# Kernel optimization log

Hardware: AMD Instinct MI355X
Metric: run time of the kernel (lower is better)

The kernel has to match this reference:

```python
import jax, jax.numpy as jnp
import numpy as np
import math

NEG = -1e9
NUM_SQUEEZE = 2


def seq_mask(lengths, max_len, dtype):
    return (jnp.arange(max_len)[None, :] < lengths[:, None]).astype(dtype)


def maximum_path(logp, attn_mask, x_lengths, y_lengths):
    """Monotonic alignment search (Viterbi DP). logp, attn_mask: [B, Tx, Ty]."""
    B, Tx, Ty = logp.shape
    logp = jnp.where(attn_mask > 0, logp, NEG)
    cols = jnp.moveaxis(logp, 2, 0)  # [Ty, B, Tx]

    v0 = jnp.where(jnp.arange(Tx)[None, :] == 0, 0.0, NEG).astype(logp.dtype)
    v0 = jnp.broadcast_to(v0, (B, Tx))

    def fwd(v, col):
        v_shift = jnp.concatenate([jnp.full((B, 1), NEG, logp.dtype), v[:, :-1]], axis=1)
        v_new = col + jnp.maximum(v, v_shift)
        return v_new, v_new

    _, values = jax.lax.scan(fwd, v0, cols)  # [Ty, B, Tx] DP table

    def bwd(index, j):
        active = j < y_lengths  # [B]
        row = jax.nn.one_hot(index, Tx, dtype=logp.dtype) * active[:, None].astype(logp.dtype)
        vprev = values[jnp.maximum(j - 1, 0)]  # [B, Tx]
        v_here = jnp.take_along_axis(vprev, index[:, None], axis=1)[:, 0]
        v_left = jnp.take_along_axis(vprev, jnp.maximum(index - 1, 0)[:, None], axis=1)[:, 0]
        dec = (index != 0) & ((index == j) | (v_here < v_left)) & active & (j > 0)
        return jnp.where(dec, index - 1, index), row

    js = jnp.arange(Ty - 1, -1, -1)
    _, rows = jax.lax.scan(bwd, x_lengths - 1, js)  # reversed j order
    path = jnp.moveaxis(jnp.flip(rows, 0), 0, 2)  # [B, Tx, Ty]
    return path * attn_mask


def setup_inputs() -> dict:
    key = jax.random.key(0)
    ks = jax.random.split(key, 6)
    B, C, Ten, Tde = 32, 80, 512, 2048
    return {
        "o_mean": jax.random.normal(ks[0], (B, C, Ten), jnp.float32),
        "o_log_scale": jax.random.normal(ks[1], (B, C, Ten), jnp.float32) * 0.1,
        "o_dur_log": jax.random.normal(ks[2], (B, 1, Ten), jnp.float32),
        "z": jax.random.normal(ks[3], (B, C, Tde), jnp.float32),
        "x_lengths": jax.random.randint(ks[4], (B,), Ten // 2, Ten + 1, jnp.int32),
        "y_lengths": jax.random.randint(ks[5], (B,), Tde // 2, Tde + 1, jnp.int32),
    }


def reference(o_mean, o_log_scale, o_dur_log, z, x_lengths, y_lengths):
    B, C, Ten = o_mean.shape
    Tde = z.shape[2]
    dt = o_mean.dtype

    # preprocess: floor y_lengths to multiple of num_squeeze
    y_lengths = (y_lengths // NUM_SQUEEZE) * NUM_SQUEEZE

    x_mask = seq_mask(x_lengths, Ten, dt)[:, None, :]   # [B,1,Tx]
    y_mask = seq_mask(y_lengths, Tde, dt)[:, None, :]   # [B,1,Ty]
    attn_mask = x_mask[:, 0, :, None] * y_mask[:, 0, None, :]  # [B,Tx,Ty]

    z = z * y_mask  # decoder output is masked

    # log-likelihood terms (torch.no_grad in original)
    o_scale = jnp.exp(-2.0 * o_log_scale)                       # [B,C,Tx]
    logp1 = jnp.sum(-0.5 * math.log(2 * math.pi) - o_log_scale, axis=1)[:, :, None]
    logp2 = jnp.einsum('bct,bcs->bts', o_scale, -0.5 * z * z)   # [B,Tx,Ty]
    logp3 = jnp.einsum('bct,bcs->bts', o_mean * o_scale, z)
    logp4 = jnp.sum(-0.5 * o_mean * o_mean * o_scale, axis=1)[:, :, None]
    logp = logp1 + logp2 + logp3 + logp4

    attn = maximum_path(logp, attn_mask, x_lengths, y_lengths)  # [B,Tx,Ty] hard path

    # compute_outputs
    y_mean = jnp.einsum('bts,bct->bcs', attn, o_mean)           # [B,C,Ty]
    y_log_scale = jnp.einsum('bts,bct->bcs', attn, o_log_scale)
    o_attn_dur = jnp.log1p(jnp.sum(attn, axis=-1))[:, None, :] * x_mask  # [B,1,Tx]

    return (
        jnp.transpose(z, (0, 2, 1)),            # z: [B,Ty,C]
        jnp.transpose(y_mean, (0, 2, 1)),       # y_mean: [B,Ty,C]
        jnp.transpose(y_log_scale, (0, 2, 1)),  # y_log_scale: [B,Ty,C]
        jnp.transpose(attn, (0, 2, 1)),         # alignments: [B,Ty,Tx]
        jnp.transpose(o_dur_log, (0, 2, 1)),    # durations_log: [B,Tx,1]
        jnp.transpose(o_attn_dur, (0, 2, 1)),   # total_durations_log: [B,Tx,1]
    )
```

## Files before the change

kernel.cpp:

```cpp
#include <hip/hip_runtime.h>
#include <math.h>

#define BB  32
#define CC  80
#define TXX 512
#define TYY 2048
#define NEGV -1e9f

__global__ __launch_bounds__(256) void k_prep(
    const float* __restrict__ om, const float* __restrict__ ols,
    float* __restrict__ SA, float* __restrict__ SB,
    float* __restrict__ L1, float* __restrict__ L4,
    float* __restrict__ OMTf, float* __restrict__ OLSTf,
    int* __restrict__ DUR)
{
    int gid = blockIdx.x * 256 + threadIdx.x;
    int b = gid >> 9, t = gid & 511;
    const float* pm = om  + (size_t)b * CC * TXX + t;
    const float* pl = ols + (size_t)b * CC * TXX + t;
    float l1 = 0.f, l4 = 0.f;
    for (int c = 0; c < CC; ++c) {
        float m  = pm[(size_t)c * TXX];
        float ls = pl[(size_t)c * TXX];
        float sa = expf(-2.0f * ls);
        l1 += (-0.9189385332046727f - ls);
        l4 += ((-0.5f * m) * m) * sa;
        SA[((size_t)b * CC + c) * TXX + t] = sa;
        SB[((size_t)b * CC + c) * TXX + t] = m * sa;
        OMTf [((size_t)b * TXX + t) * CC + c] = m;
        OLSTf[((size_t)b * TXX + t) * CC + c] = ls;
    }
    L1[gid] = l1; L4[gid] = l4; DUR[gid] = 0;
}

__global__ __launch_bounds__(256) void k_logp(
    const float* __restrict__ SA, const float* __restrict__ SB,
    const float* __restrict__ L1, const float* __restrict__ L4,
    const float* __restrict__ z,
    const int* __restrict__ xlp, const int* __restrict__ ylp,
    float* __restrict__ logp)
{
    int b = blockIdx.z;
    int ylen = (ylp[b] >> 1) << 1;
    int s0 = blockIdx.y * 128;
    if (s0 >= ylen) return;
    int t0 = blockIdx.x * 64;
    int xlen = xlp[b];
    int tid = threadIdx.x;

    __shared__ float sA[16][64], sB[16][64], sZ[16][128], sW[16][128];

    float acc2[4][8], acc3[4][8];
    #pragma unroll
    for (int i = 0; i < 4; ++i)
        #pragma unroll
        for (int j = 0; j < 8; ++j) { acc2[i][j] = 0.f; acc3[i][j] = 0.f; }

    int tt = (tid & 15) << 2;
    int ss = (tid >> 4) << 3;
    int r  = tid >> 4;
    int c4 = (tid & 15) << 2;
    int s8 = (tid & 15) << 3;

    for (int c0 = 0; c0 < CC; c0 += 16) {
        const float* pa = SA + ((size_t)b * CC + (c0 + r)) * TXX + t0 + c4;
        const float* pb = SB + ((size_t)b * CC + (c0 + r)) * TXX + t0 + c4;
        float4 va = *(const float4*)pa;
        float4 vb = *(const float4*)pb;
        *(float4*)&sA[r][c4] = va;
        *(float4*)&sB[r][c4] = vb;

        const float* pz = z + ((size_t)b * CC + (c0 + r)) * TYY + s0 + s8;
        float4 q0 = *(const float4*)pz;
        float4 q1 = *(const float4*)(pz + 4);
        float zf[8] = {q0.x, q0.y, q0.z, q0.w, q1.x, q1.y, q1.z, q1.w};
        #pragma unroll
        for (int i = 0; i < 8; ++i) {
            sZ[r][s8 + i] = zf[i];
            sW[r][s8 + i] = (-0.5f * zf[i]) * zf[i];
        }
        __syncthreads();
        #pragma unroll
        for (int kc = 0; kc < 16; ++kc) {
            float4 a2 = *(const float4*)&sA[kc][tt];
            float4 a3 = *(const float4*)&sB[kc][tt];
            float4 z0 = *(const float4*)&sZ[kc][ss];
            float4 z1 = *(const float4*)&sZ[kc][ss + 4];
            float4 w0 = *(const float4*)&sW[kc][ss];
            float4 w1 = *(const float4*)&sW[kc][ss + 4];
            float av2[4] = {a2.x, a2.y, a2.z, a2.w};
            float av3[4] = {a3.x, a3.y, a3.z, a3.w};
            float bz[8]  = {z0.x, z0.y, z0.z, z0.w, z1.x, z1.y, z1.z, z1.w};
            float bw[8]  = {w0.x, w0.y, w0.z, w0.w, w1.x, w1.y, w1.z, w1.w};
            #pragma unroll
            for (int i = 0; i < 4; ++i)
                #pragma unroll
                for (int j = 0; j < 8; ++j) {
                    acc2[i][j] = fmaf(av2[i], bw[j], acc2[i][j]);
                    acc3[i][j] = fmaf(av3[i], bz[j], acc3[i][j]);
                }
        }
        __syncthreads();
    }

    float l1a[4], l4a[4]; int bad[4];
    #pragma unroll
    for (int i = 0; i < 4; ++i) {
        int t = t0 + tt + i;
        l1a[i] = L1[b * TXX + t];
        l4a[i] = L4[b * TXX + t];
        bad[i] = (t >= xlen);
    }
    #pragma unroll
    for (int j = 0; j < 8; ++j) {
        int s = s0 + ss + j;
        float vals[4];
        #pragma unroll
        for (int i = 0; i < 4; ++i) {
            float v = ((l1a[i] + acc2[i][j]) + acc3[i][j]) + l4a[i];
            vals[i] = bad[i] ? NEGV : v;
        }
        float4 o; o.x = vals[0]; o.y = vals[1]; o.z = vals[2]; o.w = vals[3];
        *(float4*)&logp[((size_t)b * TYY + s) * TXX + t0 + tt] = o;
    }
}

__device__ __forceinline__ void dp_step(float v[8], float4 c0, float4 c1,
                                        int s_abs, int lane, unsigned char* browBase)
{
    float left = __shfl_up(v[7], 1, 64);
    if (lane == 0) left = NEGV;
    if (s_abs >= 1) {
        unsigned by = 0u;
        by |= (v[0] < left) ? 1u   : 0u;
        by |= (v[1] < v[0]) ? 2u   : 0u;
        by |= (v[2] < v[1]) ? 4u   : 0u;
        by |= (v[3] < v[2]) ? 8u   : 0u;
        by |= (v[4] < v[3]) ? 16u  : 0u;
        by |= (v[5] < v[4]) ? 32u  : 0u;
        by |= (v[6] < v[5]) ? 64u  : 0u;
        by |= (v[7] < v[6]) ? 128u : 0u;
        browBase[(size_t)(s_abs - 1) * 64] = (unsigned char)by;
    }
    float m0 = fmaxf(v[0], left);
    float m1 = fmaxf(v[1], v[0]);
    float m2 = fmaxf(v[2], v[1]);
    float m3 = fmaxf(v[3], v[2]);
    float m4 = fmaxf(v[4], v[3]);
    float m5 = fmaxf(v[5], v[4]);
    float m6 = fmaxf(v[6], v[5]);
    float m7 = fmaxf(v[7], v[6]);
    v[0] = c0.x + m0; v[1] = c0.y + m1; v[2] = c0.z + m2; v[3] = c0.w + m3;
    v[4] = c1.x + m4; v[5] = c1.y + m5; v[6] = c1.z + m6; v[7] = c1.w + m7;
}

__global__ __launch_bounds__(64) void k_fwd(
    const float* __restrict__ logp, const int* __restrict__ ylp,
    unsigned char* __restrict__ BITS)
{
    int b = blockIdx.x, lane = threadIdx.x;
    int n = (ylp[b] >> 1) << 1;
    const float* lp = logp + (size_t)b * TYY * TXX + lane * 8;
    unsigned char* brow = BITS + (size_t)b * TYY * 64 + lane;
    float v[8];
    #pragma unroll
    for (int k = 0; k < 8; ++k) v[k] = NEGV;
    if (lane == 0) v[0] = 0.0f;

    float4 p0[8], p1[8];
    #pragma unroll
    for (int i = 0; i < 8; ++i) {
        int r = (i < n) ? i : (n - 1);
        p0[i] = *(const float4*)(lp + (size_t)r * TXX);
        p1[i] = *(const float4*)(lp + (size_t)r * TXX + 4);
    }
    int s = 0;
    while (s + 8 <= n) {
        #pragma unroll
        for (int u = 0; u < 8; ++u) {
            float4 c0 = p0[u], c1 = p1[u];
            int pr = s + 8; if (pr > n - 1) pr = n - 1;
            p0[u] = *(const float4*)(lp + (size_t)pr * TXX);
            p1[u] = *(const float4*)(lp + (size_t)pr * TXX + 4);
            dp_step(v, c0, c1, s, lane, brow);
            ++s;
        }
    }
    while (s < n) {
        float4 c0 = *(const float4*)(lp + (size_t)s * TXX);
        float4 c1 = *(const float4*)(lp + (size_t)s * TXX + 4);
        dp_step(v, c0, c1, s, lane, brow);
        ++s;
    }
}

__global__ __launch_bounds__(64) void k_bwd(
    const unsigned char* __restrict__ BITS, const int* __restrict__ xlp,
    const int* __restrict__ ylp, int* __restrict__ TSTAR, int* __restrict__ DUR)
{
    int b = blockIdx.x, lane = threadIdx.x;
    int ylen = (ylp[b] >> 1) << 1;
    int xlen = xlp[b];
    const unsigned char* bb = BITS + (size_t)b * TYY * 64;
    int* tst = TSTAR + b * TYY;
    int idx = xlen - 1;
    int j0 = ylen - 1;
    while (j0 >= 0) {
        int steps = (j0 + 1 < 32) ? (j0 + 1) : 32;
        int row = j0 - 1 - lane;
        int bw = idx >> 5; if (bw > 0) --bw;
        int base_bit = bw << 5;
        unsigned w0 = 0u, w1 = 0u;
        if (lane < steps && row >= 0) {
            const unsigned* rp = (const unsigned*)(bb + (size_t)row * 64);
            w0 = rp[bw]; w1 = rp[bw + 1];
        }
        unsigned long long wq = (((unsigned long long)w1) << 32) | w0;
        int saved = 0;
        #pragma unroll
        for (int k = 0; k < 32; ++k) {
            if (k >= steps) break;
            int j = j0 - k;
            if (lane == k) saved = idx;
            unsigned long long wk = __shfl(wq, k, 64);
            unsigned bit = (unsigned)(wk >> (idx - base_bit)) & 1u;
            int dec = (idx != 0 && j > 0 && (idx == j || bit)) ? 1 : 0;
            idx -= dec;
        }
        if (lane < steps) {
            tst[j0 - lane] = saved;
            atomicAdd(&DUR[b * TXX + saved], 1);
        }
        j0 -= steps;
    }
}

__global__ __launch_bounds__(256) void k_small(
    const float* __restrict__ odur, const int* __restrict__ xlp,
    const int* __restrict__ DUR, float* __restrict__ out4,
    float* __restrict__ out5)
{
    int gid = blockIdx.x * 256 + threadIdx.x;
    int b = gid >> 9, t = gid & 511;
    out4[gid] = odur[gid];
    int xlen = xlp[b];
    float d = (float)DUR[gid];
    out5[gid] = (t < xlen) ? log1pf(d) : 0.0f;
}

__global__ __launch_bounds__(256) void k_out_sc(
    const float* __restrict__ z, const float* __restrict__ OMTf,
    const float* __restrict__ OLSTf, const int* __restrict__ TSTAR,
    const int* __restrict__ ylp,
    float* __restrict__ out0, float* __restrict__ out1,
    float* __restrict__ out2)
{
    int b = blockIdx.y;
    int s0 = blockIdx.x * 32;
    int tid = threadIdx.x;
    int ylen = (ylp[b] >> 1) << 1;
    __shared__ int sT[32];
    __shared__ float zt[32][81];
    if (tid < 32) {
        int s = s0 + tid;
        sT[tid] = (s < ylen) ? TSTAR[b * TYY + s] : 0;
    }
    int c_l = tid >> 5, s_l = tid & 31;
    #pragma unroll
    for (int cp = 0; cp < 10; ++cp) {
        int c = cp * 8 + c_l;
        zt[s_l][c] = z[((size_t)b * CC + c) * TYY + s0 + s_l];
    }
    __syncthreads();
    for (int e = tid; e < 32 * 80; e += 256) {
        int sl = e / 80;
        int cc = e - sl * 80;
        int s = s0 + sl;
        bool valid = s < ylen;
        int t = sT[sl];
        size_t o = ((size_t)b * TYY + s) * 80 + cc;
        size_t g = ((size_t)b * TXX + t) * 80 + cc;
        out0[o] = valid ? zt[sl][cc] : 0.0f;
        out1[o] = valid ? OMTf[g]    : 0.0f;
        out2[o] = valid ? OLSTf[g]   : 0.0f;
    }
}

__global__ __launch_bounds__(256) void k_attn(
    const int* __restrict__ TSTAR, const int* __restrict__ ylp,
    float* __restrict__ out3)
{
    int b = blockIdx.y;
    int s0 = blockIdx.x * 16;
    int tid = threadIdx.x;
    int ylen = (ylp[b] >> 1) << 1;
    #pragma unroll
    for (int r = 0; r < 16; ++r) {
        int s = s0 + r;
        int tr = (s < ylen) ? TSTAR[b * TYY + s] : -1;
        int t = tid << 1;
        float2 val;
        val.x = (t == tr) ? 1.0f : 0.0f;
        val.y = (t + 1 == tr) ? 1.0f : 0.0f;
        ((float2*)(out3 + ((size_t)b * TYY + s) * TXX))[tid] = val;
    }
}

extern "C" void kernel_launch(void* const* d_in, const int* in_sizes, int n_in,
                              void* d_out, int out_size, void* d_ws, size_t ws_size,
                              hipStream_t stream)
{
    const float* om   = (const float*)d_in[0];
    const float* ols  = (const float*)d_in[1];
    const float* odur = (const float*)d_in[2];
    const float* z    = (const float*)d_in[3];
    const int* xl = (const int*)d_in[4];
    const int* yl = (const int*)d_in[5];

    float* out0 = (float*)d_out;
    float* out1 = out0 + 5242880;
    float* out2 = out0 + 10485760;
    float* out3 = out0 + 15728640;
    float* out4 = out0 + 49283072;
    float* out5 = out0 + 49299456;

    float* SA   = out0;
    float* SB   = out0 + 1310720;
    float* logp = out3;

    char* ws = (char*)d_ws;
    float* L1 = (float*)ws;
    float* L4 = (float*)(ws + 65536);
    float* OMTf  = (float*)(ws + 131072);
    float* OLSTf = (float*)(ws + 5373952);
    unsigned char* BITS = (unsigned char*)(ws + 10616832);
    int* TSTAR = (int*)(ws + 14811136);
    int* DUR   = (int*)(ws + 15073280);

    hipLaunchKernelGGL(k_prep, dim3(64), dim3(256), 0, stream,
                       om, ols, SA, SB, L1, L4, OMTf, OLSTf, DUR);
    hipLaunchKernelGGL(k_logp, dim3(8, 16, 32), dim3(256), 0, stream,
                       SA, SB, L1, L4, z, xl, yl, logp);
    hipLaunchKernelGGL(k_fwd, dim3(32), dim3(64), 0, stream, logp, yl, BITS);
    hipLaunchKernelGGL(k_bwd, dim3(32), dim3(64), 0, stream, BITS, xl, yl, TSTAR, DUR);
    hipLaunchKernelGGL(k_small, dim3(64), dim3(256), 0, stream, odur, xl, DUR, out4, out5);
    hipLaunchKernelGGL(k_out_sc, dim3(64, 32), dim3(256), 0, stream,
                       z, OMTf, OLSTf, TSTAR, yl, out0, out1, out2);
    hipLaunchKernelGGL(k_attn, dim3(128, 32), dim3(256), 0, stream, TSTAR, yl, out3);
}
```

Measured before the change: 769.4 us.

## Stage prep transposes in LDS, pack FMAs, buffer DP bits and deepen prefetch

k_prep now runs on a 2D grid and stages om/ols tiles in shared memory, so the transposed OMTf/OLSTf writes become coalesced instead of strided per-thread stores. k_logp keeps its accumulators as 2-wide vectors and uses elementwise FMA, aiming at packed FP32 FMA instructions. k_fwd doubles the logp prefetch depth to 16 rows and writes the per-step decision bytes to a shared ring buffer, then flushes them to global memory as wide coalesced uint4 stores. The cost is more shared memory and more complex index handling, which adds risk at the block boundaries and in the tail loop.

```diff
diff --git a/kernel.cpp b/kernel.cpp
--- a/kernel.cpp
+++ b/kernel.cpp
@@ -6,6 +6,8 @@
 #define TXX 512
 #define TYY 2048
 #define NEGV -1e9f
+
+typedef float v2f __attribute__((ext_vector_type(2)));
 
 __global__ __launch_bounds__(256) void k_prep(
     const float* __restrict__ om, const float* __restrict__ ols,
@@ -14,23 +16,40 @@
     float* __restrict__ OMTf, float* __restrict__ OLSTf,
     int* __restrict__ DUR)
 {
-    int gid = blockIdx.x * 256 + threadIdx.x;
-    int b = gid >> 9, t = gid & 511;
-    const float* pm = om  + (size_t)b * CC * TXX + t;
-    const float* pl = ols + (size_t)b * CC * TXX + t;
-    float l1 = 0.f, l4 = 0.f;
-    for (int c = 0; c < CC; ++c) {
-        float m  = pm[(size_t)c * TXX];
-        float ls = pl[(size_t)c * TXX];
+    int b = blockIdx.y;
+    int t0 = blockIdx.x * 64;
+    int tid = threadIdx.x;
+    int cl = tid >> 6;
+    int tl = tid & 63;
+    __shared__ float sm[64][81], sl[64][81], ssa[64][81];
+    #pragma unroll
+    for (int cp = 0; cp < 20; ++cp) {
+        int c = cp * 4 + cl;
+        size_t gidx = ((size_t)b * CC + c) * TXX + t0 + tl;
+        float m = om[gidx], ls = ols[gidx];
         float sa = expf(-2.0f * ls);
-        l1 += (-0.9189385332046727f - ls);
-        l4 += ((-0.5f * m) * m) * sa;
-        SA[((size_t)b * CC + c) * TXX + t] = sa;
-        SB[((size_t)b * CC + c) * TXX + t] = m * sa;
-        OMTf [((size_t)b * TXX + t) * CC + c] = m;
-        OLSTf[((size_t)b * TXX + t) * CC + c] = ls;
-    }
-    L1[gid] = l1; L4[gid] = l4; DUR[gid] = 0;
+        SA[gidx] = sa;
+        SB[gidx] = m * sa;
+        sm[tl][c] = m; sl[tl][c] = ls; ssa[tl][c] = sa;
+    }
+    __syncthreads();
+    if (tid < 64) {
+        float l1 = 0.f, l4 = 0.f;
+        #pragma unroll 4
+        for (int c = 0; c < CC; ++c) {
+            float m = sm[tid][c], ls = sl[tid][c], sa = ssa[tid][c];
+            l1 += (-0.9189385332046727f - ls);
+            l4 += ((-0.5f * m) * m) * sa;
+        }
+        int g = b * TXX + t0 + tid;
+        L1[g] = l1; L4[g] = l4; DUR[g] = 0;
+    }
+    size_t obase = (size_t)b * TXX * CC + (size_t)t0 * CC;
+    for (int e = tid; e < 64 * CC; e += 256) {
+        int t = e / CC, c = e - t * CC;
+        OMTf[obase + e]  = sm[t][c];
+        OLSTf[obase + e] = sl[t][c];
+    }
 }
 
 __global__ __launch_bounds__(256) void k_logp(
@@ -50,11 +69,11 @@
 
     __shared__ float sA[16][64], sB[16][64], sZ[16][128], sW[16][128];
 
-    float acc2[4][8], acc3[4][8];
+    v2f acc2[4][4], acc3[4][4];
     #pragma unroll
     for (int i = 0; i < 4; ++i)
         #pragma unroll
-        for (int j = 0; j < 8; ++j) { acc2[i][j] = 0.f; acc3[i][j] = 0.f; }
+        for (int p = 0; p < 4; ++p) { acc2[i][p] = (v2f){0.f, 0.f}; acc3[i][p] = (v2f){0.f, 0.f}; }
 
     int tt = (tid & 15) << 2;
     int ss = (tid >> 4) << 3;
@@ -84,21 +103,22 @@
         for (int kc = 0; kc < 16; ++kc) {
             float4 a2 = *(const float4*)&sA[kc][tt];
             float4 a3 = *(const float4*)&sB[kc][tt];
-            float4 z0 = *(const float4*)&sZ[kc][ss];
-            float4 z1 = *(const float4*)&sZ[kc][ss + 4];
-            float4 w0 = *(const float4*)&sW[kc][ss];
-            float4 w1 = *(const float4*)&sW[kc][ss + 4];
+            const v2f* zp = (const v2f*)&sZ[kc][ss];
+            const v2f* wp = (const v2f*)&sW[kc][ss];
+            v2f bz[4] = {zp[0], zp[1], zp[2], zp[3]};
+            v2f bw[4] = {wp[0], wp[1], wp[2], wp[3]};
             float av2[4] = {a2.x, a2.y, a2.z, a2.w};
             float av3[4] = {a3.x, a3.y, a3.z, a3.w};
-            float bz[8]  = {z0.x, z0.y, z0.z, z0.w, z1.x, z1.y, z1.z, z1.w};
-            float bw[8]  = {w0.x, w0.y, w0.z, w0.w, w1.x, w1.y, w1.z, w1.w};
             #pragma unroll
-            for (int i = 0; i < 4; ++i)
+            for (int i = 0; i < 4; ++i) {
+                v2f d2 = {av2[i], av2[i]};
+                v2f d3 = {av3[i], av3[i]};
                 #pragma unroll
-                for (int j = 0; j < 8; ++j) {
-                    acc2[i][j] = fmaf(av2[i], bw[j], acc2[i][j]);
-                    acc3[i][j] = fmaf(av3[i], bz[j], acc3[i][j]);
+                for (int p = 0; p < 4; ++p) {
+                    acc2[i][p] = __builtin_elementwise_fma(d2, bw[p], acc2[i][p]);
+                    acc3[i][p] = __builtin_elementwise_fma(d3, bz[p], acc3[i][p]);
                 }
+            }
         }
         __syncthreads();
     }
@@ -112,36 +132,36 @@
         bad[i] = (t >= xlen);
     }
     #pragma unroll
-    for (int j = 0; j < 8; ++j) {
-        int s = s0 + ss + j;
-        float vals[4];
-        #pragma unroll
-        for (int i = 0; i < 4; ++i) {
-            float v = ((l1a[i] + acc2[i][j]) + acc3[i][j]) + l4a[i];
-            vals[i] = bad[i] ? NEGV : v;
-        }
-        float4 o; o.x = vals[0]; o.y = vals[1]; o.z = vals[2]; o.w = vals[3];
-        *(float4*)&logp[((size_t)b * TYY + s) * TXX + t0 + tt] = o;
-    }
-}
-
-__device__ __forceinline__ void dp_step(float v[8], float4 c0, float4 c1,
-                                        int s_abs, int lane, unsigned char* browBase)
-{
-    float left = __shfl_up(v[7], 1, 64);
-    if (lane == 0) left = NEGV;
-    if (s_abs >= 1) {
-        unsigned by = 0u;
-        by |= (v[0] < left) ? 1u   : 0u;
-        by |= (v[1] < v[0]) ? 2u   : 0u;
-        by |= (v[2] < v[1]) ? 4u   : 0u;
-        by |= (v[3] < v[2]) ? 8u   : 0u;
-        by |= (v[4] < v[3]) ? 16u  : 0u;
-        by |= (v[5] < v[4]) ? 32u  : 0u;
-        by |= (v[6] < v[5]) ? 64u  : 0u;
-        by |= (v[7] < v[6]) ? 128u : 0u;
-        browBase[(size_t)(s_abs - 1) * 64] = (unsigned char)by;
-    }
+    for (int p = 0; p < 4; ++p) {
+        #pragma unroll
+        for (int h = 0; h < 2; ++h) {
+            int s = s0 + ss + 2 * p + h;
+            float vals[4];
+            #pragma unroll
+            for (int i = 0; i < 4; ++i) {
+                float a2v = h ? acc2[i][p].y : acc2[i][p].x;
+                float a3v = h ? acc3[i][p].y : acc3[i][p].x;
+                float v = ((l1a[i] + a2v) + a3v) + l4a[i];
+                vals[i] = bad[i] ? NEGV : v;
+            }
+            float4 o; o.x = vals[0]; o.y = vals[1]; o.z = vals[2]; o.w = vals[3];
+            *(float4*)&logp[((size_t)b * TYY + s) * TXX + t0 + tt] = o;
+        }
+    }
+}
+
+__device__ __forceinline__ unsigned dp_bits(const float v[8], float left) {
+    unsigned by = (v[0] < left) ? 1u : 0u;
+    by |= (v[1] < v[0]) ? 2u   : 0u;
+    by |= (v[2] < v[1]) ? 4u   : 0u;
+    by |= (v[3] < v[2]) ? 8u   : 0u;
+    by |= (v[4] < v[3]) ? 16u  : 0u;
+    by |= (v[5] < v[4]) ? 32u  : 0u;
+    by |= (v[6] < v[5]) ? 64u  : 0u;
+    by |= (v[7] < v[6]) ? 128u : 0u;
+    return by;
+}
+__device__ __forceinline__ void dp_core(float v[8], float4 c0, float4 c1, float left) {
     float m0 = fmaxf(v[0], left);
     float m1 = fmaxf(v[1], v[0]);
     float m2 = fmaxf(v[2], v[1]);
@@ -160,37 +180,81 @@
 {
     int b = blockIdx.x, lane = threadIdx.x;
     int n = (ylp[b] >> 1) << 1;
+    int nm1 = n - 1;
     const float* lp = logp + (size_t)b * TYY * TXX + lane * 8;
-    unsigned char* brow = BITS + (size_t)b * TYY * 64 + lane;
+    unsigned char* BITSb = BITS + (size_t)b * TYY * 64;
+    __shared__ unsigned char lbits[128 * 64];
+
     float v[8];
     #pragma unroll
     for (int k = 0; k < 8; ++k) v[k] = NEGV;
     if (lane == 0) v[0] = 0.0f;
 
-    float4 p0[8], p1[8];
-    #pragma unroll
-    for (int i = 0; i < 8; ++i) {
-        int r = (i < n) ? i : (n - 1);
-        p0[i] = *(const float4*)(lp + (size_t)r * TXX);
-        p1[i] = *(const float4*)(lp + (size_t)r * TXX + 4);
-    }
-    int s = 0;
-    while (s + 8 <= n) {
-        #pragma unroll
-        for (int u = 0; u < 8; ++u) {
-            float4 c0 = p0[u], c1 = p1[u];
-            int pr = s + 8; if (pr > n - 1) pr = n - 1;
-            p0[u] = *(const float4*)(lp + (size_t)pr * TXX);
-            p1[u] = *(const float4*)(lp + (size_t)pr * TXX + 4);
-            dp_step(v, c0, c1, s, lane, brow);
-            ++s;
-        }
-    }
-    while (s < n) {
-        float4 c0 = *(const float4*)(lp + (size_t)s * TXX);
-        float4 c1 = *(const float4*)(lp + (size_t)s * TXX + 4);
-        dp_step(v, c0, c1, s, lane, brow);
-        ++s;
+    float4 p0[16], p1[16];
+    #pragma unroll
+    for (int i = 0; i < 16; ++i) {
+        int r0 = (i < nm1) ? i : nm1;
+        p0[i] = *(const float4*)(lp + (size_t)r0 * TXX);
+        p1[i] = *(const float4*)(lp + (size_t)r0 * TXX + 4);
+    }
+
+    int gs = 0;
+    for (; gs + 64 <= n; gs += 64) {
+        int hb = gs & 127;
+        unsigned char* lb_first = lbits + lane + (((hb + 127) & 127) << 6);
+        unsigned char* lb_rest  = lbits + lane + (hb << 6);
+        #pragma unroll
+        for (int j4 = 0; j4 < 4; ++j4) {
+            #pragma unroll
+            for (int uu = 0; uu < 16; ++uu) {
+                const int j = j4 * 16 + uu;
+                float4 c0 = p0[uu], c1 = p1[uu];
+                int pr = gs + j + 16; if (pr > nm1) pr = nm1;
+                p0[uu] = *(const float4*)(lp + (size_t)pr * TXX);
+                p1[uu] = *(const float4*)(lp + (size_t)pr * TXX + 4);
+                float left = __shfl_up(v[7], 1, 64);
+                if (lane == 0) left = NEGV;
+                if (j > 0 || gs > 0) {
+                    unsigned by = dp_bits(v, left);
+                    if (j == 0) *lb_first = (unsigned char)by;
+                    else        lb_rest[(j - 1) << 6] = (unsigned char)by;
+                }
+                dp_core(v, c0, c1, left);
+            }
+        }
+        if (gs >= 64) {
+            int ps = hb ^ 64;
+            const uint4* srcl = (const uint4*)(lbits + (size_t)((ps + lane) << 6));
+            uint4 q0 = srcl[0], q1 = srcl[1], q2 = srcl[2], q3 = srcl[3];
+            uint4* dstl = (uint4*)(BITSb + ((size_t)(gs - 64 + lane) << 6));
+            dstl[0] = q0; dstl[1] = q1; dstl[2] = q2; dstl[3] = q3;
+        }
+    }
+    {
+        int pbase = gs - 64;
+        int ps = pbase & 127;
+        if (lane < 63) {
+            const uint4* srcl = (const uint4*)(lbits + (size_t)((ps + lane) << 6));
+            uint4 q0 = srcl[0], q1 = srcl[1], q2 = srcl[2], q3 = srcl[3];
+            uint4* dstl = (uint4*)(BITSb + ((size_t)(pbase + lane) << 6));
+            dstl[0] = q0; dstl[1] = q1; dstl[2] = q2; dstl[3] = q3;
+        }
+    }
+    unsigned char* brow = BITSb + lane;
+    #pragma unroll
+    for (int j = 0; j < 64; ++j) {
+        int scur = gs + j;
+        if (scur >= n) break;
+        const int uu = j & 15;
+        float4 c0 = p0[uu], c1 = p1[uu];
+        int pr = scur + 16; if (pr > nm1) pr = nm1;
+        p0[uu] = *(const float4*)(lp + (size_t)pr * TXX);
+        p1[uu] = *(const float4*)(lp + (size_t)pr * TXX + 4);
+        float left = __shfl_up(v[7], 1, 64);
+        if (lane == 0) left = NEGV;
+        unsigned by = dp_bits(v, left);
+        brow[(size_t)(scur - 1) << 6] = (unsigned char)by;
+        dp_core(v, c0, c1, left);
     }
 }
 
@@ -337,7 +401,7 @@
     int* TSTAR = (int*)(ws + 14811136);
     int* DUR   = (int*)(ws + 15073280);
 
-    hipLaunchKernelGGL(k_prep, dim3(64), dim3(256), 0, stream,
+    hipLaunchKernelGGL(k_prep, dim3(8, 32), dim3(256), 0, stream,
                        om, ols, SA, SB, L1, L4, OMTf, OLSTf, DUR);
     hipLaunchKernelGGL(k_logp, dim3(8, 16, 32), dim3(256), 0, stream,
                        SA, SB, L1, L4, z, xl, yl, logp);
```

Result: slower. 808.2 us (+5.0%).
